# Kernel optimization log

Measured on AMD Instinct MI355X. Metric: run time of the kernel, lower is better.

Reference implementation:

```python
import jax, jax.numpy as jnp
import numpy as np

N_NODES = 8192
N_EDGES = 65536
IN_DIM = 768
HIDDEN = 4096
N_CLASSES = 16


def setup_inputs() -> dict:
    key = jax.random.key(0)
    k1, k2, k3, k4 = jax.random.split(key, 4)
    x = jax.random.normal(k1, (N_NODES, IN_DIM), dtype=jnp.float32)
    edge_index = jax.random.randint(k2, (2, N_EDGES), 0, N_NODES, dtype=jnp.int64)
    # Glorot-ish init scale
    W1 = jax.random.normal(k3, (IN_DIM, HIDDEN), dtype=jnp.float32) * (1.0 / np.sqrt(IN_DIM))
    b1 = jnp.zeros((HIDDEN,), dtype=jnp.float32)
    W2 = jax.random.normal(k4, (HIDDEN, N_CLASSES), dtype=jnp.float32) * (1.0 / np.sqrt(HIDDEN))
    b2 = jnp.zeros((N_CLASSES,), dtype=jnp.float32)
    return {"x": x, "edge_index": edge_index, "W1": W1, "b1": b1, "W2": W2, "b2": b2}


def reference(x, edge_index, W1, b1, W2, b2):
    # GCNConv (PyG defaults): add self-loops, symmetric deg^-1/2 normalization,
    # transform-then-aggregate, plus bias. Then ReLU -> (dropout=identity at
    # inference) -> Linear -> log_softmax.
    N = x.shape[0]
    loops = jnp.arange(N, dtype=edge_index.dtype)
    src = jnp.concatenate([edge_index[0], loops])  # [E+N]
    dst = jnp.concatenate([edge_index[1], loops])  # [E+N]

    h = x @ W1  # [N, HIDDEN] dense GEMM

    deg = jax.ops.segment_sum(jnp.ones_like(dst, dtype=h.dtype), dst, num_segments=N)
    dinv = jnp.where(deg > 0, jax.lax.rsqrt(jnp.maximum(deg, 1e-12)), 0.0)
    norm = dinv[src] * dinv[dst]  # [E+N]

    agg = jax.ops.segment_sum(h[src] * norm[:, None], dst, num_segments=N)  # [N, HIDDEN]
    h = jax.nn.relu(agg + b1)

    logits = h @ W2 + b2  # [N, N_CLASSES]
    return jax.nn.log_softmax(logits, axis=1)
```

## Files before the change

kernel.cpp:

```cpp
#include <hip/hip_runtime.h>

#define N_NODES   8192
#define N_EDGES   65536
#define IN_DIM    768
#define HIDDEN    4096
#define N_CLASSES 16
#define SLOTS     64
#define NSLAB     16

typedef unsigned short ushort_t;
typedef __attribute__((ext_vector_type(8))) short bf16x8;
typedef __attribute__((ext_vector_type(4))) float f32x4;

__device__ __forceinline__ ushort_t f2bf(float f) {
    union { float f; unsigned i; } v; v.f = f;
    unsigned r = v.i + 0x7FFFu + ((v.i >> 16) & 1u);
    return (ushort_t)(r >> 16);
}
__device__ __forceinline__ float bf2f(ushort_t u) {
    union { unsigned i; float f; } v; v.i = ((unsigned)u) << 16; return v.f;
}

#define GLD_LDS16(gp, lp) \
    __builtin_amdgcn_global_load_lds((const __attribute__((address_space(1))) void*)(gp), \
                                     (__attribute__((address_space(3))) void*)(lp), 16, 0, 0)

__device__ __forceinline__ int esrc(const int* ei, int f32mode, int e) {
    return f32mode ? ei[e] : ei[2 * e];
}
__device__ __forceinline__ int edst(const int* ei, int f32mode, int e) {
    return f32mode ? ei[N_EDGES + e] : ei[2 * N_EDGES + 2 * e];
}

__global__ __launch_bounds__(256) void phase1(const float* __restrict__ x,
                                              ushort_t* __restrict__ xbf,
                                              const float* __restrict__ W2,
                                              ushort_t* __restrict__ W2T,
                                              const int* __restrict__ ei,
                                              int* __restrict__ cnt,
                                              int* __restrict__ slots,
                                              int* __restrict__ flag) {
    int b = blockIdx.x, t = threadIdx.x;
    if (b < 16) {
        __shared__ ushort_t ld[16 * 257];
        int k0 = b * 256;
        const float4* src = (const float4*)(W2 + (long)(k0 + t) * N_CLASSES);
        #pragma unroll
        for (int j = 0; j < 4; j++) {
            float4 v = src[j];
            ld[(j * 4 + 0) * 257 + t] = f2bf(v.x);
            ld[(j * 4 + 1) * 257 + t] = f2bf(v.y);
            ld[(j * 4 + 2) * 257 + t] = f2bf(v.z);
            ld[(j * 4 + 3) * 257 + t] = f2bf(v.w);
        }
        __syncthreads();
        #pragma unroll
        for (int c = 0; c < 16; c++)
            W2T[c * HIDDEN + k0 + t] = ld[c * 257 + t];
    } else if (b < 1552) {
        long i = (long)(b - 16) * 1024 + t;
        #pragma unroll
        for (int p = 0; p < 4; p++) {
            float4 v = ((const float4*)x)[i + p * 256];
            ushort4 r = { f2bf(v.x), f2bf(v.y), f2bf(v.z), f2bf(v.w) };
            ((ushort4*)xbf)[i + p * 256] = r;
        }
    } else {
        __shared__ int sv[256];
        int v = 0;
        for (int e = t; e < 4096; e += 256) v |= ei[2 * e + 1];
        sv[t] = v;
        __syncthreads();
        for (int off = 128; off > 0; off >>= 1) {
            if (t < off) sv[t] |= sv[t + off];
            __syncthreads();
        }
        int f = (sv[0] != 0) ? 1 : 0;
        if (b == 1552 && t == 0) *flag = f;
        int e = (b - 1552) * 256 + t;
        int s = esrc(ei, f, e), d = edst(ei, f, e);
        int p = atomicAdd(&cnt[d], 1);
        if (p < SLOTS) slots[d * SLOTS + p] = s;
    }
}

#define ACC3(W_, v0_, v1_, v2_) do { \
    a[0] = fmaf(W_, bf2f(v0_.x), a[0]); a[1]  = fmaf(W_, bf2f(v0_.y), a[1]); \
    a[2] = fmaf(W_, bf2f(v0_.z), a[2]); a[3]  = fmaf(W_, bf2f(v0_.w), a[3]); \
    a[4] = fmaf(W_, bf2f(v1_.x), a[4]); a[5]  = fmaf(W_, bf2f(v1_.y), a[5]); \
    a[6] = fmaf(W_, bf2f(v1_.z), a[6]); a[7]  = fmaf(W_, bf2f(v1_.w), a[7]); \
    a[8] = fmaf(W_, bf2f(v2_.x), a[8]); a[9]  = fmaf(W_, bf2f(v2_.y), a[9]); \
    a[10] = fmaf(W_, bf2f(v2_.z), a[10]); a[11] = fmaf(W_, bf2f(v2_.w), a[11]); \
} while (0)

__global__ __launch_bounds__(256) void phase2(const float* __restrict__ W1,
                                              ushort_t* __restrict__ W1T,
                                              const ushort_t* __restrict__ xbf,
                                              const int* __restrict__ cnt,
                                              const int* __restrict__ slots,
                                              const int* __restrict__ ei,
                                              const int* __restrict__ flag,
                                              ushort_t* __restrict__ xagg) {
    __shared__ ushort_t tile[64][72];
    int b = blockIdx.x, t = threadIdx.x;
    if ((b & 3) == 3) {
        int bt = b >> 2;
        int k0 = (bt >> 6) * 64, n0 = (bt & 63) * 64;
        #pragma unroll
        for (int p = 0; p < 4; p++) {
            int k = p * 16 + (t >> 4);
            int c = (t & 15) * 4;
            float4 v = *(const float4*)(W1 + (long)(k0 + k) * HIDDEN + n0 + c);
            ushort4 r = { f2bf(v.x), f2bf(v.y), f2bf(v.z), f2bf(v.w) };
            *(ushort4*)&tile[k][c] = r;
        }
        __syncthreads();
        int n = t >> 2, kk0 = (t & 3) * 16;
        ushort_t buf[16];
        #pragma unroll
        for (int kk = 0; kk < 16; kk++) buf[kk] = tile[kk0 + kk][n];
        ushort_t* dst = W1T + (long)(n0 + n) * IN_DIM + k0 + kk0;
        *(bf16x8*)(dst)     = *(bf16x8*)&buf[0];
        *(bf16x8*)(dst + 8) = *(bf16x8*)&buf[8];
        return;
    }
    int idx = (b >> 2) * 3 + (b & 3);
    if (idx >= 2048) return;
    int w = t >> 6, l = t & 63;
    int d = idx * 4 + w;
    int fo = l * 4;
    int cd = cnt[d];
    float wd = rsqrtf((float)(cd + 1));
    float a[12];
    {
        const ushort_t* pr = xbf + (long)d * IN_DIM + fo;
        ushort4 v0 = *(const ushort4*)(pr);
        ushort4 v1 = *(const ushort4*)(pr + 256);
        ushort4 v2 = *(const ushort4*)(pr + 512);
        a[0] = wd * bf2f(v0.x); a[1]  = wd * bf2f(v0.y);
        a[2] = wd * bf2f(v0.z); a[3]  = wd * bf2f(v0.w);
        a[4] = wd * bf2f(v1.x); a[5]  = wd * bf2f(v1.y);
        a[6] = wd * bf2f(v1.z); a[7]  = wd * bf2f(v1.w);
        a[8] = wd * bf2f(v2.x); a[9]  = wd * bf2f(v2.y);
        a[10] = wd * bf2f(v2.z); a[11] = wd * bf2f(v2.w);
    }
    if (cd <= SLOTS) {
        const int* sl = slots + d * SLOTS;
        int j = 0;
        for (; j + 4 <= cd; j += 4) {
            int s0 = sl[j], s1 = sl[j + 1], s2 = sl[j + 2], s3 = sl[j + 3];
            float w0 = rsqrtf((float)(cnt[s0] + 1));
            float w1 = rsqrtf((float)(cnt[s1] + 1));
            float w2 = rsqrtf((float)(cnt[s2] + 1));
            float w3 = rsqrtf((float)(cnt[s3] + 1));
            const ushort_t* p0 = xbf + (long)s0 * IN_DIM + fo;
            const ushort_t* p1 = xbf + (long)s1 * IN_DIM + fo;
            const ushort_t* p2 = xbf + (long)s2 * IN_DIM + fo;
            const ushort_t* p3 = xbf + (long)s3 * IN_DIM + fo;
            ushort4 v00 = *(const ushort4*)(p0), v01 = *(const ushort4*)(p0 + 256), v02 = *(const ushort4*)(p0 + 512);
            ushort4 v10 = *(const ushort4*)(p1), v11 = *(const ushort4*)(p1 + 256), v12 = *(const ushort4*)(p1 + 512);
            ushort4 v20 = *(const ushort4*)(p2), v21 = *(const ushort4*)(p2 + 256), v22 = *(const ushort4*)(p2 + 512);
            ushort4 v30 = *(const ushort4*)(p3), v31 = *(const ushort4*)(p3 + 256), v32 = *(const ushort4*)(p3 + 512);
            ACC3(w0, v00, v01, v02);
            ACC3(w1, v10, v11, v12);
            ACC3(w2, v20, v21, v22);
            ACC3(w3, v30, v31, v32);
        }
        for (; j < cd; j++) {
            int s = sl[j];
            float wsv = rsqrtf((float)(cnt[s] + 1));
            const ushort_t* pp = xbf + (long)s * IN_DIM + fo;
            ushort4 u0 = *(const ushort4*)(pp), u1 = *(const ushort4*)(pp + 256), u2 = *(const ushort4*)(pp + 512);
            ACC3(wsv, u0, u1, u2);
        }
    } else {
        int f = *flag;
        for (int e = 0; e < N_EDGES; e++) {
            if (edst(ei, f, e) == d) {
                int s = esrc(ei, f, e);
                float wsv = rsqrtf((float)(cnt[s] + 1));
                const ushort_t* pp = xbf + (long)s * IN_DIM + fo;
                ushort4 u0 = *(const ushort4*)(pp), u1 = *(const ushort4*)(pp + 256), u2 = *(const ushort4*)(pp + 512);
                ACC3(wsv, u0, u1, u2);
            }
        }
    }
    ushort_t* po = xagg + (long)d * IN_DIM + fo;
    ushort4 r0 = { f2bf(a[0] * wd), f2bf(a[1] * wd), f2bf(a[2] * wd), f2bf(a[3] * wd) };
    ushort4 r1 = { f2bf(a[4] * wd), f2bf(a[5] * wd), f2bf(a[6] * wd), f2bf(a[7] * wd) };
    ushort4 r2 = { f2bf(a[8] * wd), f2bf(a[9] * wd), f2bf(a[10] * wd), f2bf(a[11] * wd) };
    *(ushort4*)(po) = r0;
    *(ushort4*)(po + 256) = r1;
    *(ushort4*)(po + 512) = r2;
}

#define FENCE() asm volatile("" ::: "memory")
#define BAR()  do { FENCE(); __builtin_amdgcn_s_barrier(); FENCE(); } while (0)
#define VMCNT(n) asm volatile("s_waitcnt vmcnt(" #n ")" ::: "memory")
#define LGKM0()  asm volatile("s_waitcnt lgkmcnt(0)" ::: "memory")
#define PRIO(x)  __builtin_amdgcn_s_setprio(x)

__global__ __launch_bounds__(512, 2) void gemm1_fused(const ushort_t* __restrict__ A,
                                                      const ushort_t* __restrict__ Bt,
                                                      const float* __restrict__ b1,
                                                      const ushort_t* __restrict__ W2T,
                                                      float* __restrict__ part) {
    __shared__ ushort_t lds[65536];
    ushort_t* ldsA = lds;
    ushort_t* ldsB = lds + 32768;

    int t = threadIdx.x;
    int w = t >> 6, l = t & 63;
    int wm = w & 3, wn = w >> 2;
    int q = l >> 4, lm = l & 15;
    int xcd = blockIdx.x & 7, j = blockIdx.x >> 3;
    int round = j >> 5, jj = j & 31;
    int by = (xcd & 3) * 4 + (jj & 3) + round * 16;
    int bx = (xcd >> 2) * 8 + (jj >> 2);
    int m0 = by * 256, n0 = bx * 256;

    int srow = t >> 3;
    int sg = (t & 7) ^ (srow & 7);
    const ushort_t* aS = A  + (long)(m0 + srow) * IN_DIM + sg * 8;
    const ushort_t* bS = Bt + (long)(n0 + srow) * IN_DIM + sg * 8;

#define STAGE_A(B_, h, ko) do { \
    GLD_LDS16(aS + (h) * 128 * IN_DIM + (ko),              ldsA + (B_) * 16384 + (h) * 8192 + w * 512); \
    GLD_LDS16(aS + ((h) * 128 + 64) * IN_DIM + (ko),       ldsA + (B_) * 16384 + (h) * 8192 + 4096 + w * 512); \
} while (0)
#define STAGE_B(B_, h, ko) do { \
    GLD_LDS16(bS + (h) * 128 * IN_DIM + (ko),              ldsB + (B_) * 16384 + (h) * 8192 + w * 512); \
    GLD_LDS16(bS + ((h) * 128 + 64) * IN_DIM + (ko),       ldsB + (B_) * 16384 + (h) * 8192 + 4096 + w * 512); \
} while (0)
#define LDA(dst, qm, B_) do { \
    const ushort_t* p_ = ldsA + (B_) * 16384 + (wm * 64 + (qm) * 32 + lm) * 64; \
    int x0_ = ((q) ^ (lm & 7)) * 8, x1_ = ((4 + q) ^ (lm & 7)) * 8; \
    dst[0][0] = *(const bf16x8*)(p_ + x0_);        dst[0][1] = *(const bf16x8*)(p_ + x1_); \
    dst[1][0] = *(const bf16x8*)(p_ + 1024 + x0_); dst[1][1] = *(const bf16x8*)(p_ + 1024 + x1_); \
} while (0)
#define LDB(dst, qn, B_) do { \
    const ushort_t* p_ = ldsB + (B_) * 16384 + (wn * 128 + (qn) * 64 + lm) * 64; \
    int x0_ = ((q) ^ (lm & 7)) * 8, x1_ = ((4 + q) ^ (lm & 7)) * 8; \
    dst[0][0] = *(const bf16x8*)(p_ + x0_);        dst[0][1] = *(const bf16x8*)(p_ + x1_); \
    dst[1][0] = *(const bf16x8*)(p_ + 1024 + x0_); dst[1][1] = *(const bf16x8*)(p_ + 1024 + x1_); \
    dst[2][0] = *(const bf16x8*)(p_ + 2048 + x0_); dst[2][1] = *(const bf16x8*)(p_ + 2048 + x1_); \
    dst[3][0] = *(const bf16x8*)(p_ + 3072 + x0_); dst[3][1] = *(const bf16x8*)(p_ + 3072 + x1_); \
} while (0)
#define MFMAQ(qm, qn, a_, b_) do { \
    _Pragma("unroll") for (int j_ = 0; j_ < 2; j_++) \
    _Pragma("unroll") for (int nt_ = 0; nt_ < 4; nt_++) \
    _Pragma("unroll") for (int mt_ = 0; mt_ < 2; mt_++) \
        acc[(qm) * 2 + mt_][(qn) * 4 + nt_] = __builtin_amdgcn_mfma_f32_16x16x32_bf16( \
            a_[mt_][j_], b_[nt_][j_], acc[(qm) * 2 + mt_][(qn) * 4 + nt_], 0, 0, 0); \
} while (0)

    int kA = 0, kB = 0;
    STAGE_A(0, 0, kA); STAGE_A(0, 1, kA); kA += 64;
    STAGE_B(0, 0, kB); STAGE_B(0, 1, kB); kB += 64;
    STAGE_A(1, 0, kA); STAGE_A(1, 1, kA); kA += 64;

    bf16x8 aq0[2][2], aq1[2][2], bq0[4][2], bq1[4][2];
    f32x4 acc[4][8] = {};

    VMCNT(4);
    BAR();

    #pragma unroll 1
    for (int it = 0; it < 5; ++it) {
        LDA(aq0, 0, 0); LDB(bq0, 0, 0); STAGE_B(1, 0, kB);
        BAR(); LGKM0(); PRIO(1); MFMAQ(0, 0, aq0, bq0); PRIO(0); BAR();
        LDA(aq1, 1, 0); STAGE_B(1, 1, kB); kB += 64;
        BAR(); LGKM0(); PRIO(1); MFMAQ(1, 0, aq1, bq0); PRIO(0); BAR();
        LDB(bq1, 1, 0); STAGE_A(0, 0, kA);
        BAR(); LGKM0(); PRIO(1); MFMAQ(1, 1, aq1, bq1); PRIO(0); BAR();
        STAGE_A(0, 1, kA); kA += 64;
        VMCNT(4);
        BAR(); PRIO(1); MFMAQ(0, 1, aq0, bq1); PRIO(0); BAR();
        LDA(aq0, 0, 1); LDB(bq0, 0, 1); STAGE_B(0, 0, kB);
        BAR(); LGKM0(); PRIO(1); MFMAQ(0, 0, aq0, bq0); PRIO(0); BAR();
        LDA(aq1, 1, 1); STAGE_B(0, 1, kB); kB += 64;
        BAR(); LGKM0(); PRIO(1); MFMAQ(1, 0, aq1, bq0); PRIO(0); BAR();
        LDB(bq1, 1, 1); STAGE_A(1, 0, kA);
        BAR(); LGKM0(); PRIO(1); MFMAQ(1, 1, aq1, bq1); PRIO(0); BAR();
        STAGE_A(1, 1, kA); kA += 64;
        VMCNT(4);
        BAR(); PRIO(1); MFMAQ(0, 1, aq0, bq1); PRIO(0); BAR();
    }
    LDA(aq0, 0, 0); LDB(bq0, 0, 0); STAGE_B(1, 0, kB);
    BAR(); LGKM0(); PRIO(1); MFMAQ(0, 0, aq0, bq0); PRIO(0); BAR();
    LDA(aq1, 1, 0); STAGE_B(1, 1, kB);
    BAR(); LGKM0(); PRIO(1); MFMAQ(1, 0, aq1, bq0); PRIO(0); BAR();
    LDB(bq1, 1, 0);
    BAR(); LGKM0(); PRIO(1); MFMAQ(1, 1, aq1, bq1); PRIO(0); BAR();
    VMCNT(0);
    BAR(); PRIO(1); MFMAQ(0, 1, aq0, bq1); PRIO(0); BAR();
    LDA(aq0, 0, 1); LDB(bq0, 0, 1);
    BAR(); LGKM0(); PRIO(1); MFMAQ(0, 0, aq0, bq0); PRIO(0); BAR();
    LDA(aq1, 1, 1);
    BAR(); LGKM0(); PRIO(1); MFMAQ(1, 0, aq1, bq0); PRIO(0); BAR();
    LDB(bq1, 1, 1);
    BAR(); LGKM0(); PRIO(1); MFMAQ(1, 1, aq1, bq1); PRIO(0); BAR();
    PRIO(1); MFMAQ(0, 1, aq0, bq1); PRIO(0);

    float bias[8];
    #pragma unroll
    for (int ng = 0; ng < 8; ng++) bias[ng] = b1[n0 + wn * 128 + ng * 16 + lm];
    bf16x8 w2f[2][2];
    #pragma unroll
    for (int eh = 0; eh < 2; eh++)
        #pragma unroll
        for (int kk = 0; kk < 2; kk++)
            w2f[eh][kk] = *(const bf16x8*)(W2T + (long)lm * HIDDEN + n0 + wn * 128 + eh * 64 + kk * 32 + q * 8);

    __syncthreads();
    ushort_t* slab = lds + w * 4096;
    f32x4 acc2[4] = {};
    #pragma unroll
    for (int eh = 0; eh < 2; eh++) {
        #pragma unroll
        for (int mg = 0; mg < 4; mg++)
            #pragma unroll
            for (int nt = 0; nt < 4; nt++) {
                int gc = nt * 2 + (lm >> 3);
                #pragma unroll
                for (int rr = 0; rr < 4; rr++) {
                    int row = mg * 16 + q * 4 + rr;
                    float v = acc[mg][eh * 4 + nt][rr] + bias[eh * 4 + nt];
                    v = v > 0.0f ? v : 0.0f;
                    slab[row * 64 + ((gc ^ (row & 7)) * 8) + (lm & 7)] = f2bf(v);
                }
            }
        #pragma unroll
        for (int kk = 0; kk < 2; kk++)
            #pragma unroll
            for (int mt2 = 0; mt2 < 4; mt2++) {
                bf16x8 a2 = *(const bf16x8*)(slab + (mt2 * 16 + lm) * 64 + (((kk * 4 + q) ^ (lm & 7)) * 8));
                acc2[mt2] = __builtin_amdgcn_mfma_f32_16x16x32_bf16(a2, w2f[eh][kk], acc2[mt2], 0, 0, 0);
            }
    }

    __syncthreads();
    float* psum = (float*)lds;
    if (wn == 1) {
        #pragma unroll
        for (int mt2 = 0; mt2 < 4; mt2++)
            #pragma unroll
            for (int rr = 0; rr < 4; rr++)
                psum[(wm * 64 + mt2 * 16 + q * 4 + rr) * 17 + lm] = acc2[mt2][rr];
    }
    __syncthreads();
    if (wn == 0) {
        float* pslab = part + ((long)bx * N_NODES + m0 + wm * 64) * N_CLASSES;
        #pragma unroll
        for (int mt2 = 0; mt2 < 4; mt2++)
            #pragma unroll
            for (int rr = 0; rr < 4; rr++) {
                int row = mt2 * 16 + q * 4 + rr;
                pslab[row * N_CLASSES + lm] = acc2[mt2][rr] + psum[(wm * 64 + row) * 17 + lm];
            }
    }
#undef STAGE_A
#undef STAGE_B
#undef LDA
#undef LDB
#undef MFMAQ
}

__global__ __launch_bounds__(256) void reduce_softmax(const float* __restrict__ part,
                                                      const float* __restrict__ b2,
                                                      float* __restrict__ out) {
    int t = threadIdx.x;
    int row = blockIdx.x * 16 + (t >> 4);
    int cls = t & 15;
    float v = b2[cls];
    #pragma unroll
    for (int s = 0; s < NSLAB; s++)
        v += part[((long)s * N_NODES + row) * N_CLASSES + cls];
    float mx = v;
    #pragma unroll
    for (int off = 1; off < 16; off <<= 1)
        mx = fmaxf(mx, __shfl_xor(mx, off, 64));
    float e = __expf(v - mx);
    float sm = e;
    #pragma unroll
    for (int off = 1; off < 16; off <<= 1)
        sm += __shfl_xor(sm, off, 64);
    out[(long)row * N_CLASSES + cls] = v - mx - __logf(sm);
}


extern "C" void kernel_launch(void* const* d_in, const int* in_sizes, int n_in,
                              void* d_out, int out_size, void* d_ws, size_t ws_size,
                              hipStream_t stream) {
    const float* x  = (const float*)d_in[0];
    const int*   ei = (const int*)d_in[1];
    const float* W1 = (const float*)d_in[2];
    const float* b1 = (const float*)d_in[3];
    const float* W2 = (const float*)d_in[4];
    const float* b2 = (const float*)d_in[5];
    float* out = (float*)d_out;
    char* ws = (char*)d_ws;

    float*    part  = (float*)(ws);
    ushort_t* xagg  = (ushort_t*)(ws + 16777216);
    ushort_t* xbf   = (ushort_t*)(ws + 29360128);
    ushort_t* W1T   = (ushort_t*)(ws + 41943040);
    ushort_t* W2T   = (ushort_t*)(ws + 48234496);
    int*      cnt   = (int*)(ws + 48365568);
    int*      slots = (int*)(ws + 48398336);
    int*      flag  = (int*)(ws + 50495488);

    hipMemsetAsync(cnt, 0, 32768, stream);
    phase1<<<1808, 256, 0, stream>>>(x, xbf, W2, W2T, ei, cnt, slots, flag);
    phase2<<<3072, 256, 0, stream>>>(W1, W1T, xbf, cnt, slots, ei, flag, xagg);
    gemm1_fused<<<(N_NODES / 256) * (HIDDEN / 256), 512, 0, stream>>>(xagg, W1T, b1, W2T, part);
    reduce_softmax<<<N_NODES / 16, 256, 0, stream>>>(part, b2, out);
}
```

Baseline: 162.8 us.

## Bucket edges per destination block in LDS, move W1 transpose into prep kernel

```diff
diff --git a/kernel.cpp b/kernel.cpp
--- a/kernel.cpp
+++ b/kernel.cpp
@@ -32,17 +32,20 @@
     return f32mode ? ei[N_EDGES + e] : ei[2 * N_EDGES + 2 * e];
 }
 
-__global__ __launch_bounds__(256) void phase1(const float* __restrict__ x,
-                                              ushort_t* __restrict__ xbf,
-                                              const float* __restrict__ W2,
-                                              ushort_t* __restrict__ W2T,
-                                              const int* __restrict__ ei,
-                                              int* __restrict__ cnt,
-                                              int* __restrict__ slots,
-                                              int* __restrict__ flag) {
+__global__ __launch_bounds__(256) void prep(const float* __restrict__ x,
+                                            ushort_t* __restrict__ xbf,
+                                            const float* __restrict__ W1,
+                                            ushort_t* __restrict__ W1T,
+                                            const float* __restrict__ W2,
+                                            ushort_t* __restrict__ W2T,
+                                            const int* __restrict__ ei,
+                                            int* __restrict__ cnt,
+                                            int* __restrict__ slots,
+                                            int* __restrict__ flag) {
+    __shared__ char smem[34816];
     int b = blockIdx.x, t = threadIdx.x;
     if (b < 16) {
-        __shared__ ushort_t ld[16 * 257];
+        ushort_t* ld = (ushort_t*)smem;
         int k0 = b * 256;
         const float4* src = (const float4*)(W2 + (long)(k0 + t) * N_CLASSES);
         #pragma unroll
@@ -65,8 +68,31 @@
             ushort4 r = { f2bf(v.x), f2bf(v.y), f2bf(v.z), f2bf(v.w) };
             ((ushort4*)xbf)[i + p * 256] = r;
         }
+    } else if (b < 2320) {
+        ushort_t (*tile)[72] = (ushort_t(*)[72])smem;
+        int bt = b - 1552;
+        int k0 = (bt >> 6) * 64, n0 = (bt & 63) * 64;
+        #pragma unroll
+        for (int p = 0; p < 4; p++) {
+            int k = p * 16 + (t >> 4);
+            int c = (t & 15) * 4;
+            float4 v = *(const float4*)(W1 + (long)(k0 + k) * HIDDEN + n0 + c);
+            ushort4 r = { f2bf(v.x), f2bf(v.y), f2bf(v.z), f2bf(v.w) };
+            *(ushort4*)&tile[k][c] = r;
+        }
+        __syncthreads();
+        int n = t >> 2, kk0 = (t & 3) * 16;
+        ushort_t buf[16];
+        #pragma unroll
+        for (int kk = 0; kk < 16; kk++) buf[kk] = tile[kk0 + kk][n];
+        ushort_t* dst = W1T + (long)(n0 + n) * IN_DIM + k0 + kk0;
+        *(bf16x8*)(dst)     = *(bf16x8*)&buf[0];
+        *(bf16x8*)(dst + 8) = *(bf16x8*)&buf[8];
     } else {
-        __shared__ int sv[256];
+        int* scnt = (int*)smem;
+        unsigned short* sslot = (unsigned short*)(smem + 1024);
+        int* sv = (int*)(smem + 33792);
+        scnt[t] = 0;
         int v = 0;
         for (int e = t; e < 4096; e += 256) v |= ei[2 * e + 1];
         sv[t] = v;
@@ -76,11 +102,21 @@
             __syncthreads();
         }
         int f = (sv[0] != 0) ? 1 : 0;
-        if (b == 1552 && t == 0) *flag = f;
-        int e = (b - 1552) * 256 + t;
-        int s = esrc(ei, f, e), d = edst(ei, f, e);
-        int p = atomicAdd(&cnt[d], 1);
-        if (p < SLOTS) slots[d * SLOTS + p] = s;
+        int d0 = (b - 2320) * 256;
+        if (b == 2320 && t == 0) *flag = f;
+        for (int e = t; e < N_EDGES; e += 256) {
+            int dd = edst(ei, f, e);
+            unsigned r = (unsigned)(dd - d0);
+            if (r < 256u) {
+                int ss = esrc(ei, f, e);
+                int p = atomicAdd(&scnt[r], 1);
+                if (p < SLOTS) sslot[r * SLOTS + p] = (unsigned short)ss;
+            }
+        }
+        __syncthreads();
+        cnt[d0 + t] = scnt[t];
+        for (int i = t; i < 256 * SLOTS; i += 256)
+            slots[d0 * SLOTS + i] = (int)sslot[i];
     }
 }
 
@@ -93,41 +129,15 @@
     a[10] = fmaf(W_, bf2f(v2_.z), a[10]); a[11] = fmaf(W_, bf2f(v2_.w), a[11]); \
 } while (0)
 
-__global__ __launch_bounds__(256) void phase2(const float* __restrict__ W1,
-                                              ushort_t* __restrict__ W1T,
-                                              const ushort_t* __restrict__ xbf,
-                                              const int* __restrict__ cnt,
-                                              const int* __restrict__ slots,
-                                              const int* __restrict__ ei,
-                                              const int* __restrict__ flag,
-                                              ushort_t* __restrict__ xagg) {
-    __shared__ ushort_t tile[64][72];
-    int b = blockIdx.x, t = threadIdx.x;
-    if ((b & 3) == 3) {
-        int bt = b >> 2;
-        int k0 = (bt >> 6) * 64, n0 = (bt & 63) * 64;
-        #pragma unroll
-        for (int p = 0; p < 4; p++) {
-            int k = p * 16 + (t >> 4);
-            int c = (t & 15) * 4;
-            float4 v = *(const float4*)(W1 + (long)(k0 + k) * HIDDEN + n0 + c);
-            ushort4 r = { f2bf(v.x), f2bf(v.y), f2bf(v.z), f2bf(v.w) };
-            *(ushort4*)&tile[k][c] = r;
-        }
-        __syncthreads();
-        int n = t >> 2, kk0 = (t & 3) * 16;
-        ushort_t buf[16];
-        #pragma unroll
-        for (int kk = 0; kk < 16; kk++) buf[kk] = tile[kk0 + kk][n];
-        ushort_t* dst = W1T + (long)(n0 + n) * IN_DIM + k0 + kk0;
-        *(bf16x8*)(dst)     = *(bf16x8*)&buf[0];
-        *(bf16x8*)(dst + 8) = *(bf16x8*)&buf[8];
-        return;
-    }
-    int idx = (b >> 2) * 3 + (b & 3);
-    if (idx >= 2048) return;
+__global__ __launch_bounds__(256) void aggregate(const ushort_t* __restrict__ xbf,
+                                                 const int* __restrict__ cnt,
+                                                 const int* __restrict__ slots,
+                                                 const int* __restrict__ ei,
+                                                 const int* __restrict__ flag,
+                                                 ushort_t* __restrict__ xagg) {
+    int t = threadIdx.x;
     int w = t >> 6, l = t & 63;
-    int d = idx * 4 + w;
+    int d = blockIdx.x * 4 + w;
     int fo = l * 4;
     int cd = cnt[d];
     float wd = rsqrtf((float)(cd + 1));
@@ -410,9 +420,8 @@
     int*      slots = (int*)(ws + 48398336);
     int*      flag  = (int*)(ws + 50495488);
 
-    hipMemsetAsync(cnt, 0, 32768, stream);
-    phase1<<<1808, 256, 0, stream>>>(x, xbf, W2, W2T, ei, cnt, slots, flag);
-    phase2<<<3072, 256, 0, stream>>>(W1, W1T, xbf, cnt, slots, ei, flag, xagg);
+    prep<<<2352, 256, 0, stream>>>(x, xbf, W1, W1T, W2, W2T, ei, cnt, slots, flag);
+    aggregate<<<2048, 256, 0, stream>>>(xbf, cnt, slots, ei, flag, xagg);
     gemm1_fused<<<(N_NODES / 256) * (HIDDEN / 256), 512, 0, stream>>>(xagg, W1T, b1, W2T, part);
     reduce_softmax<<<N_NODES / 16, 256, 0, stream>>>(part, b2, out);
 }
```

Measured after the change: 278.5 us. 71.1% more time.
